# Kernel tuning notes

Measured on AMD Instinct MI355X. Metric: run time of the kernel, lower is better.

## Reference

```python
import jax, jax.numpy as jnp
import numpy as np

D_MODEL = 1024
N_HEAD = 16
D_K = D_MODEL // N_HEAD
B, S = 4, 2048


def setup_inputs() -> dict:
    key = jax.random.key(0)
    ks = jax.random.split(key, 12)
    def w(k):
        return jax.random.normal(k, (D_MODEL, D_MODEL), dtype=jnp.float32) * 0.02
    def b(k):
        return jax.random.normal(k, (D_MODEL,), dtype=jnp.float32) * 0.02
    return {
        "x": jax.random.normal(ks[0], (B, S, D_MODEL), dtype=jnp.float32),
        "pos_emb": jax.random.normal(ks[1], (S, D_MODEL), dtype=jnp.float32),
        "Wq": w(ks[2]), "bq": b(ks[3]),
        "Wk": w(ks[4]), "bk": b(ks[5]),
        "Wv": w(ks[6]), "bv": b(ks[7]),
        "Wp": w(ks[8]), "bp": b(ks[9]),
        "Wo": w(ks[10]), "bo": b(ks[11]),
    }


def reference(x, pos_emb, Wq, bq, Wk, bk, Wv, bv, Wp, bp, Wo, bo):
    # x: [B, S, D]; pos_emb: [S, D]. cache=None path (prefill): kv_len == S.
    Bsz, Sl, _ = x.shape
    def heads(t):  # [B, S, D] -> [B, H, S, dk]
        return t.reshape(Bsz, Sl, N_HEAD, D_K).transpose(0, 2, 1, 3)
    q = heads(x @ Wq.T + bq)
    k = heads(x @ Wk.T + bk)
    v = heads(x @ Wv.T + bv)
    # pos projection: [S, D] -> [H, S, dk]
    p = (pos_emb @ Wp.T + bp).reshape(Sl, N_HEAD, D_K).transpose(1, 0, 2)
    q_pos = q + p[None]  # broadcast over batch
    scores = jnp.einsum("bhqd,bhkd->bhqk", q_pos, k) / jnp.sqrt(jnp.asarray(D_K, x.dtype))
    # causal mask: triu(ones(S, S), diagonal=1) positions are masked
    causal = jnp.tril(jnp.ones((Sl, Sl), dtype=bool))  # True = keep
    scores = jnp.where(causal[None, None], scores, -jnp.inf)
    attn = jax.nn.softmax(scores, axis=-1)  # dropout is identity (eval / p=0)
    out = jnp.einsum("bhqk,bhkd->bhqd", attn, v)
    out = out.transpose(0, 2, 1, 3).reshape(Bsz, Sl, D_MODEL)
    return out @ Wo.T + bo
```

## Files before the change

### kernel.cpp

```cpp
#include <hip/hip_runtime.h>

#define D_MODEL 1024
#define N_HEADS 16
#define DK 64
#define BATCH 4
#define SEQ 2048
#define MROWS (BATCH * SEQ)
#define TILE_E (256 * 64)

typedef float f32x4 __attribute__((ext_vector_type(4)));
typedef short bf16x8 __attribute__((ext_vector_type(8)));
typedef unsigned short u16;
typedef unsigned short u16x8 __attribute__((ext_vector_type(8)));

__device__ __forceinline__ float bf2f(u16 u) {
    union { unsigned int i; float f; } v; v.i = ((unsigned int)u) << 16; return v.f;
}
__device__ __forceinline__ u16 f2bf(float f) {
    union { float f; unsigned int i; } v; v.f = f;
    unsigned int u = v.i;
    u += 0x7fffu + ((u >> 16) & 1u);
    return (u16)(u >> 16);
}
__device__ __forceinline__ unsigned int pk2(float a, float b) {
    union { float f; unsigned int i; } ua, ub; ua.f = a; ub.f = b;
    return __builtin_amdgcn_perm(ub.i + 0x8000u, ua.i + 0x8000u, 0x07060302u);
}

typedef unsigned int u32_as1 __attribute__((address_space(1)));
typedef unsigned int u32_as3 __attribute__((address_space(3)));
__device__ __forceinline__ void gload16(const u16* g, u16* l) {
    __builtin_amdgcn_global_load_lds((const u32_as1*)g, (u32_as3*)l, 16, 0, 0);
}

__global__ __launch_bounds__(256) void convert_all(
    const float* __restrict__ x, const float* __restrict__ pe,
    const float* __restrict__ w0, const float* __restrict__ w1, const float* __restrict__ w2,
    const float* __restrict__ w3, const float* __restrict__ w4,
    u16* __restrict__ xb, u16* __restrict__ pb,
    u16* __restrict__ wb0, u16* __restrict__ wb1, u16* __restrict__ wb2,
    u16* __restrict__ wb3, u16* __restrict__ wb4)
{
    int t = blockIdx.x * 256 + threadIdx.x;
    const float* src; u16* dst; int idx;
    if (t < 1048576)      { src = x;  dst = xb; idx = t; }
    else if (t < 1310720) { src = pe; dst = pb; idx = t - 1048576; }
    else {
        int r = t - 1310720; int w = r >> 17; idx = r & 131071;
        if      (w == 0) { src = w0; dst = wb0; }
        else if (w == 1) { src = w1; dst = wb1; }
        else if (w == 2) { src = w2; dst = wb2; }
        else if (w == 3) { src = w3; dst = wb3; }
        else             { src = w4; dst = wb4; }
    }
    const float4* p = (const float4*)src + (size_t)idx * 2;
    float4 a = p[0], b = p[1];
    u16x8 o;
    o[0] = f2bf(a.x); o[1] = f2bf(a.y); o[2] = f2bf(a.z); o[3] = f2bf(a.w);
    o[4] = f2bf(b.x); o[5] = f2bf(b.y); o[6] = f2bf(b.z); o[7] = f2bf(b.w);
    *((u16x8*)dst + idx) = o;
}

#define SA(bufp, h, kk) do { \
    gload16(Ag + (size_t)((h) * 64) * 1024 + (kk),       (bufp) + ((h) * 64 + wv * 8) * 64); \
    gload16(Ag + (size_t)((h) * 64 + 128) * 1024 + (kk), (bufp) + ((h) * 64 + 128 + wv * 8) * 64); \
} while (0)
#define SB(bufp, h, kk) do { \
    gload16(Wg + (size_t)((h) * 32) * 1024 + (kk),       (bufp) + (wq2 * 64 + (h) * 32 + w3 * 8) * 64); \
    gload16(Wg + (size_t)((h) * 32 + 128) * 1024 + (kk), (bufp) + (128 + wq2 * 64 + (h) * 32 + w3 * 8) * 64); \
} while (0)
#define LOAD_A(mh) \
    _Pragma("unroll") \
    for (int mi = 0; mi < 4; ++mi) { \
        aA[mi][0] = *(const bf16x8*)&Abuf[aoff0 + ((mh) * 64 + mi * 16) * 64]; \
        aA[mi][1] = *(const bf16x8*)&Abuf[aoff1 + ((mh) * 64 + mi * 16) * 64]; \
    }
#define LOAD_B(nh) \
    _Pragma("unroll") \
    for (int ni = 0; ni < 2; ++ni) { \
        bB[nh][ni][0] = *(const bf16x8*)&Bbuf[boff0 + ((nh) * 32 + ni * 16) * 64]; \
        bB[nh][ni][1] = *(const bf16x8*)&Bbuf[boff1 + ((nh) * 32 + ni * 16) * 64]; \
    }
#define MFMA16(mh, nh) \
    _Pragma("unroll") \
    for (int ks = 0; ks < 2; ++ks) \
        _Pragma("unroll") \
        for (int mi = 0; mi < 4; ++mi) \
            _Pragma("unroll") \
            for (int ni = 0; ni < 2; ++ni) \
                acc[(mh) * 4 + mi][(nh) * 2 + ni] = __builtin_amdgcn_mfma_f32_16x16x32_bf16( \
                    aA[mi][ks], bB[nh][ni][ks], acc[(mh) * 4 + mi][(nh) * 2 + ni], 0, 0, 0);

__device__ __forceinline__ void gemm256_loop(
    const u16* __restrict__ Ag, const u16* __restrict__ Wg,
    u16* AsBase, u16* BsBase, int wv,
    int aoff0, int aoff1, int boff0, int boff1, f32x4 (&acc)[8][4])
{
    const int wq2 = wv >> 2, w3 = wv & 3;
    bf16x8 aA[4][2], bB[2][2][2];

    SA(AsBase, 0, 0); SB(BsBase, 0, 0); SB(BsBase, 1, 0); SA(AsBase, 1, 0);
    SA(AsBase + TILE_E, 0, 64); SB(BsBase + TILE_E, 0, 64); SA(AsBase + TILE_E, 1, 64);
    asm volatile("s_waitcnt vmcnt(6)" ::: "memory");
    __builtin_amdgcn_s_barrier();

    for (int T = 0; T < 16; ++T) {
        u16* Abuf = AsBase + (T & 1) * TILE_E;
        u16* Bbuf = BsBase + (T & 1) * TILE_E;
        u16* Both = BsBase + ((T & 1) ^ 1) * TILE_E;
        const int k2 = T * 64 + 128;

        LOAD_A(0); LOAD_B(0);
        if (T < 15) SB(Both, 1, T * 64 + 64);
        __builtin_amdgcn_s_barrier();
        asm volatile("s_waitcnt lgkmcnt(0)" ::: "memory");
        __builtin_amdgcn_s_setprio(1); MFMA16(0, 0); __builtin_amdgcn_s_setprio(0);
        __builtin_amdgcn_s_barrier();

        LOAD_B(1);
        if (T < 14) SA(Abuf, 0, k2);
        __builtin_amdgcn_s_barrier();
        asm volatile("s_waitcnt lgkmcnt(0)" ::: "memory");
        __builtin_amdgcn_s_setprio(1); MFMA16(0, 1); __builtin_amdgcn_s_setprio(0);
        __builtin_amdgcn_s_barrier();

        LOAD_A(1);
        if (T < 14) SB(Bbuf, 0, k2);
        __builtin_amdgcn_s_barrier();
        asm volatile("s_waitcnt lgkmcnt(0)" ::: "memory");
        __builtin_amdgcn_s_setprio(1); MFMA16(1, 0); __builtin_amdgcn_s_setprio(0);
        __builtin_amdgcn_s_barrier();

        if (T < 14) SA(Abuf, 1, k2);
        __builtin_amdgcn_s_barrier();
        __builtin_amdgcn_s_setprio(1); MFMA16(1, 1); __builtin_amdgcn_s_setprio(0);
        if (T < 14)      { asm volatile("s_waitcnt vmcnt(6)" ::: "memory"); }
        else if (T < 15) { asm volatile("s_waitcnt vmcnt(0)" ::: "memory"); }
        __builtin_amdgcn_s_barrier();
    }
}

__global__ __launch_bounds__(512, 2) void qkv_gemm256(
    const u16* __restrict__ xb, const u16* __restrict__ peb,
    const u16* __restrict__ wqb, const u16* __restrict__ wkb,
    const u16* __restrict__ wvb, const u16* __restrict__ wpb,
    const float* __restrict__ bq, const float* __restrict__ bk,
    const float* __restrict__ bv, const float* __restrict__ bp,
    u16* __restrict__ Qb, u16* __restrict__ Kb, u16* __restrict__ V3,
    u16* __restrict__ Pb)
{
    __shared__ __align__(16) u16 SH[4 * TILE_E];
    u16* As = SH;
    u16* Bs = SH + 2 * TILE_E;

    const int tid  = threadIdx.x;
    const int lane = tid & 63;
    const int wv   = tid >> 6;
    const int l15  = lane & 15;
    const int quad = lane >> 4;
    const int wm = wv >> 2, wn = wv & 3;

    int wg = (blockIdx.x & 7) * 52 + (blockIdx.x >> 3);
    int chunk, m0, n0;
    if (wg < 384) {
        int g = wg >> 5;
        chunk = g >> 2; n0 = (g & 3) * 256; m0 = (wg & 31) * 256;
    } else {
        int r = wg - 384;
        chunk = 3; n0 = (r >> 3) * 256; m0 = (r & 7) * 256;
    }

    const u16* Abase = (chunk == 3) ? peb : xb;
    const u16* Wbase = (chunk == 0) ? wqb : ((chunk == 1) ? wkb : ((chunk == 2) ? wvb : wpb));

    const int trow = tid >> 3;
    const int swz  = ((tid & 7) ^ (trow & 7)) * 8;
    const u16* Ag = Abase + (size_t)(m0 + trow) * 1024 + swz;
    const u16* Wg = Wbase + (size_t)(n0 + (wv >> 2) * 64 + (trow & 31)) * 1024 + swz;

    const int x7 = l15 & 7;
    const int aoff0 = (wm * 128 + l15) * 64 + ((quad    ) ^ x7) * 8;
    const int aoff1 = (wm * 128 + l15) * 64 + ((quad + 4) ^ x7) * 8;
    const int boff0 = (wn * 64 + l15) * 64 + ((quad    ) ^ x7) * 8;
    const int boff1 = (wn * 64 + l15) * 64 + ((quad + 4) ^ x7) * 8;

    f32x4 acc[8][4];
#pragma unroll
    for (int i = 0; i < 8; ++i)
#pragma unroll
        for (int j = 0; j < 4; ++j) acc[i][j] = f32x4{0.f, 0.f, 0.f, 0.f};

    gemm256_loop(Ag, Wg, As, Bs, wv, aoff0, aoff1, boff0, boff1, acc);

    const float* bias = (chunk == 0) ? bq : ((chunk == 1) ? bk : ((chunk == 2) ? bv : bp));
    const int r0 = quad * 4;
    if (chunk == 2) {
#pragma unroll
        for (int n = 0; n < 4; ++n) {
            int col = n0 + wn * 64 + n * 16 + l15;
            float bvv = bias[col];
#pragma unroll
            for (int m = 0; m < 8; ++m) {
                int row0 = m0 + wm * 128 + m * 16 + r0;
                int hh = col >> 6, d = col & 63;
                int bb = row0 >> 11, sl = row0 & 2047;
                union { u16 h[4]; uint2 v; } pk;
#pragma unroll
                for (int r = 0; r < 4; ++r) pk.h[r] = f2bf(acc[m][n][r] + bvv);
                *((uint2*)V3 + ((size_t)(bb * 16 + hh) * 512 + (sl >> 2)) * 64 + d) = pk.v;
            }
        }
    } else {
        u16* dst = (chunk == 0) ? Qb : ((chunk == 1) ? Kb : Pb);
#pragma unroll
        for (int p = 0; p < 2; ++p) {
            __syncthreads();
            if (wm == p) {
#pragma unroll
                for (int n = 0; n < 4; ++n) {
                    int colL = wn * 64 + n * 16 + l15;
                    float bvv = bias[n0 + colL];
#pragma unroll
                    for (int m = 0; m < 8; ++m) {
#pragma unroll
                        for (int r = 0; r < 4; ++r)
                            SH[(m * 16 + r0 + r) * 264 + colL] = f2bf(acc[m][n][r] + bvv);
                    }
                }
            }
            __syncthreads();
            const int rbase = m0 + p * 128;
#pragma unroll
            for (int s = 0; s < 2; ++s) {
                int rowL = (tid >> 3) + s * 64;
#pragma unroll
                for (int i = 0; i < 4; ++i) {
                    int cc = (tid & 7) + i * 8;
                    *(u16x8*)(dst + (size_t)(rbase + rowL) * 1024 + n0 + cc * 8) =
                        *(const u16x8*)&SH[rowL * 264 + cc * 8];
                }
            }
        }
    }
}

#undef SA
#undef SB
#undef LOAD_A
#undef LOAD_B
#undef MFMA16

__global__ __launch_bounds__(256) void gemm_out(
    const u16* __restrict__ A, const u16* __restrict__ W,
    const float* __restrict__ bias, float* __restrict__ Cout)
{
    __shared__ __align__(16) u16 As[128 * 32];
    __shared__ __align__(16) u16 Bs[128 * 32];

    const int tid  = threadIdx.x;
    const int lane = tid & 63;
    const int wv   = tid >> 6;
    const int l15  = lane & 15;
    const int quad = lane >> 4;
    const int m0   = blockIdx.x * 128;
    const int n0   = blockIdx.y * 128;
    const int wrow = (wv >> 1) * 64;
    const int wcol = (wv & 1) * 64;

    f32x4 acc[4][4];
#pragma unroll
    for (int i = 0; i < 4; ++i)
#pragma unroll
        for (int j = 0; j < 4; ++j) acc[i][j] = f32x4{0.f, 0.f, 0.f, 0.f};

    const int lr = lane >> 2;
    const int lc = (lane & 3) * 8;
    const u16* Ag = A + (size_t)(m0 + wv * 16 + lr) * 1024 + lc;
    const u16* Wg = W + (size_t)(n0 + wv * 16 + lr) * 1024 + lc;
    u16* Al = &As[wv * 16 * 32];
    u16* Bl = &Bs[wv * 16 * 32];

    for (int k0 = 0; k0 < 1024; k0 += 32) {
        __syncthreads();
        gload16(Ag + k0, Al);
        gload16(Ag + 64 * 1024 + k0, Al + 64 * 32);
        gload16(Wg + k0, Bl);
        gload16(Wg + 64 * 1024 + k0, Bl + 64 * 32);
        __syncthreads();

        bf16x8 af[4], bfr[4];
#pragma unroll
        for (int i = 0; i < 4; ++i)
            af[i] = *(const bf16x8*)&As[(wrow + 16 * i + l15) * 32 + quad * 8];
#pragma unroll
        for (int j = 0; j < 4; ++j)
            bfr[j] = *(const bf16x8*)&Bs[(wcol + 16 * j + l15) * 32 + quad * 8];
#pragma unroll
        for (int i = 0; i < 4; ++i)
#pragma unroll
            for (int j = 0; j < 4; ++j)
                acc[i][j] = __builtin_amdgcn_mfma_f32_16x16x32_bf16(af[i], bfr[j], acc[i][j], 0, 0, 0);
    }

    const int r0 = quad * 4;
#pragma unroll
    for (int i = 0; i < 4; ++i)
#pragma unroll
        for (int j = 0; j < 4; ++j) {
            int col = n0 + wcol + 16 * j + l15;
            float bvv = bias[col];
#pragma unroll
            for (int r = 0; r < 4; ++r) {
                int row = m0 + wrow + 16 * i + r0 + r;
                Cout[(size_t)row * 1024 + col] = acc[i][j][r] + bvv;
            }
        }
}

__global__ __launch_bounds__(512, 4) void flash_attn_mfma(
    const u16* __restrict__ Q, const u16* __restrict__ Kq,
    const u16* __restrict__ V3, const u16* __restrict__ Pb, u16* __restrict__ O)
{
    __shared__ __align__(16) u16 Ks[2][64 * 72];
    __shared__ __align__(16) u16 Vs[2][64 * 72];

    const int tid  = threadIdx.x;
    const int lane = tid & 63;
    const int wv   = tid >> 6;
    const int l15  = lane & 15;
    const int quad = lane >> 4;
    const int j    = blockIdx.y;
    const int h    = blockIdx.x & 15;
    const int b    = blockIdx.x >> 4;
    const int qblk = (wv < 4) ? j : (15 - j);
    const int wq0  = qblk * 128 + (wv & 3) * 32;

    bf16x8 qf[2][2];
    const size_t qrowbase = (size_t)(b * SEQ) * D_MODEL + h * DK;
#pragma unroll
    for (int qb = 0; qb < 2; ++qb)
#pragma unroll
        for (int ks = 0; ks < 2; ++ks) {
            int qrow = wq0 + qb * 16 + l15;
            u16x8 qr = *(const u16x8*)(Q + qrowbase + (size_t)qrow * D_MODEL + ks * 32 + quad * 8);
            u16x8 pr = *(const u16x8*)(Pb + (size_t)qrow * D_MODEL + h * DK + ks * 32 + quad * 8);
            u16x8 o;
#pragma unroll
            for (int t = 0; t < 8; ++t)
                o[t] = f2bf((bf2f(qr[t]) + bf2f(pr[t])) * 0.180336880111120f);
            qf[qb][ks] = *(bf16x8*)&o;
        }

    f32x4 Oacc[2][4];
#pragma unroll
    for (int i = 0; i < 2; ++i)
#pragma unroll
        for (int jj = 0; jj < 4; ++jj) Oacc[i][jj] = f32x4{0.f, 0.f, 0.f, 0.f};
    float l_r[2] = {0.f, 0.f};

    const int sr  = tid >> 3;
    const int c   = tid & 7;
    const int sc8 = c * 8;
    const int vs0 = (c >> 2) * 32 + ((2 * c)     & 3) * 8 + ((c >> 1) & 1) * 4;
    const int vs1 = (c >> 2) * 32 + ((2 * c + 1) & 3) * 8 + ((c >> 1) & 1) * 4;
    const u16* Kg = Kq + (size_t)(b * SEQ + sr) * D_MODEL + h * DK + sc8;
    const uint2* Vg = (const uint2*)V3 + ((size_t)(b * 16 + h) * 512 + c * 2) * 64 + sr;
    u16x8 kreg = *(const u16x8*)Kg;
    uint2 v0 = Vg[0], v1 = Vg[64];

    *(u16x8*)&Ks[0][sr * 72 + sc8] = kreg;
    *(uint2*)&Vs[0][sr * 72 + vs0] = v0;
    *(uint2*)&Vs[0][sr * 72 + vs1] = v1;
    __syncthreads();

    const int ktmaxb = 31 - 2 * j;
    for (int kt = 0; kt <= ktmaxb; ++kt) {
        const int cur = kt & 1;
        if (kt < ktmaxb) {
            kreg = *(const u16x8*)(Kg + (size_t)(kt + 1) * 64 * D_MODEL);
            v0 = Vg[(size_t)(kt + 1) * 1024];
            v1 = Vg[(size_t)(kt + 1) * 1024 + 64];
        }

        if (kt * 64 <= wq0 + 31) {
            f32x4 sacc[4][2];
#pragma unroll
            for (int kb = 0; kb < 4; ++kb)
#pragma unroll
                for (int qb = 0; qb < 2; ++qb) sacc[kb][qb] = f32x4{0.f, 0.f, 0.f, 0.f};
            __builtin_amdgcn_s_setprio(1);
#pragma unroll
            for (int ks = 0; ks < 2; ++ks) {
                bf16x8 kf[4];
#pragma unroll
                for (int kb = 0; kb < 4; ++kb)
                    kf[kb] = *(const bf16x8*)&Ks[cur][(kb * 16 + l15) * 72 + ks * 32 + quad * 8];
#pragma unroll
                for (int kb = 0; kb < 4; ++kb)
#pragma unroll
                    for (int qb = 0; qb < 2; ++qb)
                        sacc[kb][qb] = __builtin_amdgcn_mfma_f32_16x16x32_bf16(kf[kb], qf[qb][ks], sacc[kb][qb], 0, 0, 0);
            }
            __builtin_amdgcn_s_setprio(0);

            if (kt * 64 + 63 > wq0) {
#pragma unroll
                for (int kb = 0; kb < 4; ++kb) {
                    int key_g = kt * 64 + kb * 16 + quad * 4;
#pragma unroll
                    for (int qb = 0; qb < 2; ++qb) {
                        int q_g = wq0 + qb * 16 + l15;
#pragma unroll
                        for (int r = 0; r < 4; ++r)
                            if (key_g + r > q_g) sacc[kb][qb][r] = -1e30f;
                    }
                }
            }

            bf16x8 pf[2][2];
#pragma unroll
            for (int qb = 0; qb < 2; ++qb) {
                float s = 0.f;
                float p[4][4];
#pragma unroll
                for (int kb = 0; kb < 4; ++kb) {
                    p[kb][0] = __builtin_amdgcn_exp2f(sacc[kb][qb][0]);
                    p[kb][1] = __builtin_amdgcn_exp2f(sacc[kb][qb][1]);
                    p[kb][2] = __builtin_amdgcn_exp2f(sacc[kb][qb][2]);
                    p[kb][3] = __builtin_amdgcn_exp2f(sacc[kb][qb][3]);
                    s += (p[kb][0] + p[kb][1]) + (p[kb][2] + p[kb][3]);
                }
                l_r[qb] += s;
#pragma unroll
                for (int ks = 0; ks < 2; ++ks) {
                    union { unsigned int w[4]; bf16x8 v; } u;
                    u.w[0] = pk2(p[2 * ks][0],     p[2 * ks][1]);
                    u.w[1] = pk2(p[2 * ks][2],     p[2 * ks][3]);
                    u.w[2] = pk2(p[2 * ks + 1][0], p[2 * ks + 1][1]);
                    u.w[3] = pk2(p[2 * ks + 1][2], p[2 * ks + 1][3]);
                    pf[qb][ks] = u.v;
                }
            }

            __builtin_amdgcn_s_setprio(1);
#pragma unroll
            for (int ks = 0; ks < 2; ++ks) {
                bf16x8 vf[4];
#pragma unroll
                for (int db = 0; db < 4; ++db)
                    vf[db] = *(const bf16x8*)&Vs[cur][(db * 16 + l15) * 72 + ks * 32 + quad * 8];
#pragma unroll
                for (int qb = 0; qb < 2; ++qb)
#pragma unroll
                    for (int db = 0; db < 4; ++db)
                        Oacc[qb][db] = __builtin_amdgcn_mfma_f32_16x16x32_bf16(pf[qb][ks], vf[db], Oacc[qb][db], 0, 0, 0);
            }
            __builtin_amdgcn_s_setprio(0);
        }

        if (kt < ktmaxb) {
            *(u16x8*)&Ks[cur ^ 1][sr * 72 + sc8] = kreg;
            *(uint2*)&Vs[cur ^ 1][sr * 72 + vs0] = v0;
            *(uint2*)&Vs[cur ^ 1][sr * 72 + vs1] = v1;
        }
        __syncthreads();
    }

    float linv[2];
#pragma unroll
    for (int qb = 0; qb < 2; ++qb) {
        float s = l_r[qb];
        s += __shfl_xor(s, 16);
        s += __shfl_xor(s, 32);
        linv[qb] = 1.f / s;
    }
#pragma unroll
    for (int qb = 0; qb < 2; ++qb)
#pragma unroll
        for (int r = 0; r < 4; ++r) {
            float li = __shfl(linv[qb], quad * 4 + r);
            size_t row = (size_t)(b * SEQ + wq0 + qb * 16 + quad * 4 + r) * D_MODEL + h * DK;
#pragma unroll
            for (int db = 0; db < 4; ++db)
                O[row + db * 16 + l15] = f2bf(Oacc[qb][db][r] * li);
        }
}

extern "C" void kernel_launch(void* const* d_in, const int* in_sizes, int n_in,
                              void* d_out, int out_size, void* d_ws, size_t ws_size,
                              hipStream_t stream) {
    const float* x  = (const float*)d_in[0];
    const float* pe = (const float*)d_in[1];
    const float* Wq = (const float*)d_in[2];  const float* bq = (const float*)d_in[3];
    const float* Wk = (const float*)d_in[4];  const float* bk = (const float*)d_in[5];
    const float* Wv = (const float*)d_in[6];  const float* bv = (const float*)d_in[7];
    const float* Wp = (const float*)d_in[8];  const float* bp = (const float*)d_in[9];
    const float* Wo = (const float*)d_in[10]; const float* bo = (const float*)d_in[11];
    float* out = (float*)d_out;
    char* ws = (char*)d_ws;

    size_t off = 0;
    u16* xb  = (u16*)(ws + off); off += (size_t)MROWS * D_MODEL * 2;
    u16* peb = (u16*)(ws + off); off += (size_t)SEQ * D_MODEL * 2;
    u16* wqb = (u16*)(ws + off); off += (size_t)D_MODEL * D_MODEL * 2;
    u16* wkb = (u16*)(ws + off); off += (size_t)D_MODEL * D_MODEL * 2;
    u16* wvb = (u16*)(ws + off); off += (size_t)D_MODEL * D_MODEL * 2;
    u16* wpb = (u16*)(ws + off); off += (size_t)D_MODEL * D_MODEL * 2;
    u16* wob = (u16*)(ws + off); off += (size_t)D_MODEL * D_MODEL * 2;
    u16* Qb  = (u16*)(ws + off); off += (size_t)MROWS * D_MODEL * 2;
    u16* Kb  = (u16*)(ws + off); off += (size_t)MROWS * D_MODEL * 2;
    u16* V3b = (u16*)(ws + off); off += (size_t)MROWS * D_MODEL * 2;
    u16* Pb  = (u16*)(ws + off); off += (size_t)SEQ * D_MODEL * 2;
    u16* AO = xb;

    convert_all<<<7680, 256, 0, stream>>>(x, pe, Wq, Wk, Wv, Wp, Wo,
                                          xb, peb, wqb, wkb, wvb, wpb, wob);

    qkv_gemm256<<<416, 512, 0, stream>>>(
        xb, peb, wqb, wkb, wvb, wpb, bq, bk, bv, bp, Qb, Kb, V3b, Pb);

    flash_attn_mfma<<<dim3(64, 8), 512, 0, stream>>>(Qb, Kb, V3b, Pb, AO);

    gemm_out<<<dim3(64, 8), 256, 0, stream>>>(AO, wob, bo, out);
}
```

Measured before the change: 265.4 us.

## Split causal flash attention into 256-thread blocks, one per query block

The attention kernel previously paired a short and a long causal query block inside one 512-thread workgroup to balance work. It now launches twice as many 256-thread workgroups, each handling a single 128-row query block, ordered longest-first, and loops only over the K/V tiles that block needs. K/V staging is reworked so each thread loads twice as much data per tile. This lets the scheduler balance uneven causal work across CUs and lets short blocks finish early, at the cost of more total K/V tile loads per head and more per-thread staging registers.

```diff
diff --git a/kernel.cpp b/kernel.cpp
--- a/kernel.cpp
+++ b/kernel.cpp
@@ -317,7 +317,7 @@
         }
 }
 
-__global__ __launch_bounds__(512, 4) void flash_attn_mfma(
+__global__ __launch_bounds__(256, 4) void flash_attn_mfma(
     const u16* __restrict__ Q, const u16* __restrict__ Kq,
     const u16* __restrict__ V3, const u16* __restrict__ Pb, u16* __restrict__ O)
 {
@@ -329,11 +329,12 @@
     const int wv   = tid >> 6;
     const int l15  = lane & 15;
     const int quad = lane >> 4;
-    const int j    = blockIdx.y;
-    const int h    = blockIdx.x & 15;
-    const int b    = blockIdx.x >> 4;
-    const int qblk = (wv < 4) ? j : (15 - j);
-    const int wq0  = qblk * 128 + (wv & 3) * 32;
+    const int gg   = blockIdx.x;
+    const int h    = gg & 15;
+    const int b    = gg >> 4;
+    const int y    = 15 - (int)blockIdx.y;
+    const int wq0  = y * 128 + wv * 32;
+    const int NT   = 2 * y + 2;
 
     bf16x8 qf[2][2];
     const size_t qrowbase = (size_t)(b * SEQ) * D_MODEL + h * DK;
@@ -358,28 +359,41 @@
         for (int jj = 0; jj < 4; ++jj) Oacc[i][jj] = f32x4{0.f, 0.f, 0.f, 0.f};
     float l_r[2] = {0.f, 0.f};
 
-    const int sr  = tid >> 3;
-    const int c   = tid & 7;
-    const int sc8 = c * 8;
-    const int vs0 = (c >> 2) * 32 + ((2 * c)     & 3) * 8 + ((c >> 1) & 1) * 4;
-    const int vs1 = (c >> 2) * 32 + ((2 * c + 1) & 3) * 8 + ((c >> 1) & 1) * 4;
+    const int sr  = tid >> 2;
+    const int sc8 = (tid & 3) * 16;
     const u16* Kg = Kq + (size_t)(b * SEQ + sr) * D_MODEL + h * DK + sc8;
-    const uint2* Vg = (const uint2*)V3 + ((size_t)(b * 16 + h) * 512 + c * 2) * 64 + sr;
-    u16x8 kreg = *(const u16x8*)Kg;
-    uint2 v0 = Vg[0], v1 = Vg[64];
-
-    *(u16x8*)&Ks[0][sr * 72 + sc8] = kreg;
-    *(uint2*)&Vs[0][sr * 72 + vs0] = v0;
-    *(uint2*)&Vs[0][sr * 72 + vs1] = v1;
+
+    const uint2* Vgp = (const uint2*)V3 + (size_t)gg * 32768 + tid;
+    const int vd = tid & 63;
+    int vb[4];
+#pragma unroll
+    for (int i = 0; i < 4; ++i) {
+        int g16 = (tid >> 6) + 4 * i;
+        vb[i] = (g16 >> 3) * 32 + (g16 & 3) * 8 + ((g16 >> 2) & 1) * 4;
+    }
+
+    u16x8 kr0 = *(const u16x8*)Kg;
+    u16x8 kr1 = *(const u16x8*)(Kg + 8);
+    uint2 vr0 = Vgp[0], vr1 = Vgp[256], vr2 = Vgp[512], vr3 = Vgp[768];
+
+    *(u16x8*)&Ks[0][sr * 72 + sc8]     = kr0;
+    *(u16x8*)&Ks[0][sr * 72 + sc8 + 8] = kr1;
+    *(uint2*)&Vs[0][vd * 72 + vb[0]] = vr0;
+    *(uint2*)&Vs[0][vd * 72 + vb[1]] = vr1;
+    *(uint2*)&Vs[0][vd * 72 + vb[2]] = vr2;
+    *(uint2*)&Vs[0][vd * 72 + vb[3]] = vr3;
     __syncthreads();
 
-    const int ktmaxb = 31 - 2 * j;
-    for (int kt = 0; kt <= ktmaxb; ++kt) {
+    for (int kt = 0; kt < NT; ++kt) {
         const int cur = kt & 1;
-        if (kt < ktmaxb) {
-            kreg = *(const u16x8*)(Kg + (size_t)(kt + 1) * 64 * D_MODEL);
-            v0 = Vg[(size_t)(kt + 1) * 1024];
-            v1 = Vg[(size_t)(kt + 1) * 1024 + 64];
+        if (kt + 1 < NT) {
+            const u16* Kn = Kg + (size_t)(kt + 1) * 64 * D_MODEL;
+            kr0 = *(const u16x8*)Kn;
+            kr1 = *(const u16x8*)(Kn + 8);
+            vr0 = Vgp[(size_t)(kt + 1) * 1024];
+            vr1 = Vgp[(size_t)(kt + 1) * 1024 + 256];
+            vr2 = Vgp[(size_t)(kt + 1) * 1024 + 512];
+            vr3 = Vgp[(size_t)(kt + 1) * 1024 + 768];
         }
 
         if (kt * 64 <= wq0 + 31) {
@@ -458,10 +472,13 @@
             __builtin_amdgcn_s_setprio(0);
         }
 
-        if (kt < ktmaxb) {
-            *(u16x8*)&Ks[cur ^ 1][sr * 72 + sc8] = kreg;
-            *(uint2*)&Vs[cur ^ 1][sr * 72 + vs0] = v0;
-            *(uint2*)&Vs[cur ^ 1][sr * 72 + vs1] = v1;
+        if (kt + 1 < NT) {
+            *(u16x8*)&Ks[cur ^ 1][sr * 72 + sc8]     = kr0;
+            *(u16x8*)&Ks[cur ^ 1][sr * 72 + sc8 + 8] = kr1;
+            *(uint2*)&Vs[cur ^ 1][vd * 72 + vb[0]] = vr0;
+            *(uint2*)&Vs[cur ^ 1][vd * 72 + vb[1]] = vr1;
+            *(uint2*)&Vs[cur ^ 1][vd * 72 + vb[2]] = vr2;
+            *(uint2*)&Vs[cur ^ 1][vd * 72 + vb[3]] = vr3;
         }
         __syncthreads();
     }
@@ -519,7 +536,7 @@
     qkv_gemm256<<<416, 512, 0, stream>>>(
         xb, peb, wqb, wkb, wvb, wpb, bq, bk, bv, bp, Qb, Kb, V3b, Pb);
 
-    flash_attn_mfma<<<dim3(64, 8), 512, 0, stream>>>(Qb, Kb, V3b, Pb, AO);
+    flash_attn_mfma<<<dim3(64, 16), 256, 0, stream>>>(Qb, Kb, V3b, Pb, AO);
 
     gemm_out<<<dim3(64, 8), 256, 0, stream>>>(AO, wob, bo, out);
 }
```

Measured after the change: 260.7 us. No clear change (-1.8%).
